# Performance work log

Hardware: AMD Instinct MI355X
Metric: run time of the kernel (lower is better)

Reference implementation:

```python
import jax, jax.numpy as jnp
import numpy as np

B, N, D, H, L, K, V = 2, 2048, 512, 8, 4, 32, 256
HD = D // H
MOD = 4294967296.0
SCALE = 1.0 / np.sqrt(HD)


def _ln(x, g, b):
    m = x.mean(-1, keepdims=True)
    v = ((x - m) ** 2).mean(-1, keepdims=True)
    return (x - m) * jax.lax.rsqrt(v + 1e-5) * g + b


def _expmap0(v, c):
    sc = jnp.sqrt(c)
    vn = jnp.maximum(jnp.linalg.norm(v, axis=-1, keepdims=True), 1e-8)
    return jnp.tanh(sc * vn) * v / (sc * vn)


def _knn_poincare(pos, c):
    xx = jnp.sum(pos ** 2, -1)                                    # [N]
    d2 = jnp.maximum(xx[:, None] + xx[None, :] - 2.0 * pos @ pos.T, 0.0)
    denom = (1.0 - c * xx)[:, None] * (1.0 - c * xx)[None, :] + 1e-8
    arg = jnp.maximum(1.0 + 2.0 * c * d2 / denom, 1.0)
    dist = jnp.arccosh(arg) / jnp.sqrt(c)                         # [N,N]
    neg_d, idx = jax.lax.top_k(-dist, K)                          # smallest-k
    return -neg_d, idx                                            # [N,K],[N,K]


def _forward(hashes, indices, emb, hash_proj, Wb, bb, log_c, pos_tangent,
             Wq, bq, Wk, bk, Wv, bv, Wo, bo, W1, b1, W2, b2,
             g1, be1, g2, be2, log_tau, Wout, bout):
    c = jnp.exp(log_c)
    char = emb[indices]                                           # [B,N,D]
    he = (hashes[..., None].astype(jnp.float32) / MOD) @ hash_proj  # [B,N,D]
    x = jnp.concatenate([char, he], -1) @ Wb + bb                 # [B,N,D]

    # kNN structure computed under no_grad in the original
    pos = _expmap0(jax.lax.stop_gradient(pos_tangent), jax.lax.stop_gradient(c))
    attn_dists, idx = _knn_poincare(pos, jax.lax.stop_gradient(c))  # shared over batch

    for i in range(L):
        xn = _ln(x, g1[i], be1[i])
        q = (xn @ Wq[i] + bq[i]).reshape(B, N, H, HD).transpose(0, 2, 1, 3)
        k = (xn @ Wk[i] + bk[i]).reshape(B, N, H, HD).transpose(0, 2, 1, 3)
        v = (xn @ Wv[i] + bv[i]).reshape(B, N, H, HD).transpose(0, 2, 1, 3)
        kg = k[:, :, idx, :]                                      # [B,H,N,K,HD]
        vg = v[:, :, idx, :]
        fs = jnp.einsum('bhnd,bhnkd->bhnk', q, kg) * SCALE
        gs = -attn_dists[None, None] / (jnp.exp(log_tau[i]) + 1e-8)
        p = jax.nn.softmax(fs + gs, axis=-1)                      # [B,H,N,K]
        ao = jnp.einsum('bhnk,bhnkd->bhnd', p, vg)
        ao = ao.transpose(0, 2, 1, 3).reshape(B, N, D)
        x = x + ao @ Wo[i] + bo[i]
        xn2 = _ln(x, g2[i], be2[i])
        x = x + jax.nn.gelu(xn2 @ W1[i] + b1[i], approximate=False) @ W2[i] + b2[i]

    return x[:, -1, :] @ Wout + bout                              # [B,V]


def setup_inputs():
    key = jax.random.key(0)
    ks = jax.random.split(key, 20)
    rn = lambda k, s, sc=0.02: jax.random.normal(k, s, jnp.float32) * sc
    z = lambda s: jnp.zeros(s, jnp.float32)
    o = lambda s: jnp.ones(s, jnp.float32)
    return {
        'hashes': jax.random.randint(ks[0], (B, N), 0, 1000000),
        'indices': jax.random.randint(ks[1], (B, N), 0, V),
        'emb': rn(ks[2], (V, D)),
        'hash_proj': rn(ks[3], (1, D)),
        'Wb': rn(ks[4], (2 * D, D)),
        'bb': z((D,)),
        'log_c': jnp.array(0.0, jnp.float32),
        'pos_tangent': rn(ks[5], (N, D)),
        'Wq': rn(ks[6], (L, D, D)), 'bq': z((L, D)),
        'Wk': rn(ks[7], (L, D, D)), 'bk': z((L, D)),
        'Wv': rn(ks[8], (L, D, D)), 'bv': z((L, D)),
        'Wo': rn(ks[9], (L, D, D)), 'bo': z((L, D)),
        'W1': rn(ks[10], (L, D, 4 * D)), 'b1': z((L, 4 * D)),
        'W2': rn(ks[11], (L, 4 * D, D)), 'b2': z((L, D)),
        'g1': o((L, D)), 'be1': z((L, D)),
        'g2': o((L, D)), 'be2': z((L, D)),
        'log_tau': z((L,)),
        'Wout': rn(ks[12], (D, V)), 'bout': z((V,)),
    }


def reference(hashes, indices, emb, hash_proj, Wb, bb, log_c, pos_tangent,
              Wq, bq, Wk, bk, Wv, bv, Wo, bo, W1, b1, W2, b2,
              g1, be1, g2, be2, log_tau, Wout, bout):
    return _forward(hashes, indices, emb, hash_proj, Wb, bb, log_c, pos_tangent,
                    Wq, bq, Wk, bk, Wv, bv, Wo, bo, W1, b1, W2, b2,
                    g1, be1, g2, be2, log_tau, Wout, bout)
```

## Files before the change

### kernel.cpp

```cpp
#include <hip/hip_runtime.h>
#include <hip/hip_bf16.h>
#include <math.h>

#define Bb 2
#define Nn 2048
#define Dd 512
#define Hh 8
#define Ll 4
#define Kk 32
#define Vv 256
#define HDh 64
#define Mrows (Bb*Nn)

static constexpr float SCALE_QK = 0.125f;
static constexpr float INV_MOD = 1.0f / 4294967296.0f;

typedef _Float16 f16;
typedef _Float16 f16x8 __attribute__((ext_vector_type(8)));
typedef _Float16 f16x4 __attribute__((ext_vector_type(4)));
typedef _Float16 f16x2 __attribute__((ext_vector_type(2)));
typedef float f32x4 __attribute__((ext_vector_type(4)));
typedef unsigned long long u64;

#define AS_GLOBAL(p) ((const __attribute__((address_space(1))) void*)(p))
#define AS_LDS(p)    ((__attribute__((address_space(3))) void*)(p))
__device__ __forceinline__ void gload16(const f16* g, f16* l) {
    __builtin_amdgcn_global_load_lds(AS_GLOBAL(g), AS_LDS(l), 16, 0, 0);
}

__global__ __launch_bounds__(256)
void prep_kernel(const float* __restrict__ log_c, const float* __restrict__ log_tau,
                 float* __restrict__ scal,
                 const float* __restrict__ bq, const float* __restrict__ bk,
                 const float* __restrict__ bv, float* __restrict__ bqkv,
                 const float* __restrict__ emb, f16* __restrict__ emb16) {
    int id = blockIdx.x * 256 + threadIdx.x;
    if (id < Vv * Dd) emb16[id] = (f16)emb[id];
    if (id < Ll * 1536) {
        int l = id / 1536, r = id % 1536;
        const float* src = (r < 512) ? bq : ((r < 1024) ? bk : bv);
        bqkv[id] = src[l * 512 + (r & 511)];
    }
    if (id == 0) {
        float c = expf(log_c[0]);
        scal[0] = c;
        scal[1] = sqrtf(c);
    }
    if (id < Ll) scal[2 + id] = 1.0f / (expf(log_tau[id]) + 1e-8f);
}

__global__ __launch_bounds__(256)
void hvec_part_kernel(const float* __restrict__ hash_proj,
                      const float* __restrict__ Wb,
                      float* __restrict__ part) {
    const int b = blockIdx.x;
    const int t = threadIdx.x;
    float a0 = 0.f, a1 = 0.f;
#pragma unroll
    for (int i = 0; i < 16; i++) {
        int kx = b * 16 + i;
        float hp = hash_proj[kx];
        const float* wr = Wb + (size_t)(Dd + kx) * Dd;
        a0 = fmaf(hp, wr[t], a0);
        a1 = fmaf(hp, wr[t + 256], a1);
    }
    part[b * Dd + t]       = a0;
    part[b * Dd + t + 256] = a1;
}
__global__ __launch_bounds__(256)
void hvec_red_kernel(const float* __restrict__ part, float* __restrict__ hvec) {
    const int n = blockIdx.x * 256 + threadIdx.x;
    float acc = 0.f;
#pragma unroll
    for (int b = 0; b < 32; b++) acc += part[b * Dd + n];
    hvec[n] = acc;
}

__global__ __launch_bounds__(256)
void trans_kernel(const float* __restrict__ src, f16* __restrict__ dst,
                  int K, int N, long sStride, long dStride) {
    __shared__ float tile[32][33];
    const float* s = src + blockIdx.z * sStride;
    f16* d = dst + blockIdx.z * dStride;
    int k0 = blockIdx.y * 32, n0 = blockIdx.x * 32;
    int tx = threadIdx.x & 31, ty = threadIdx.x >> 5;
#pragma unroll
    for (int i = 0; i < 32; i += 8)
        tile[ty + i][tx] = s[(long)(k0 + ty + i) * N + n0 + tx];
    __syncthreads();
#pragma unroll
    for (int i = 0; i < 32; i += 8)
        d[(long)(n0 + ty + i) * K + k0 + tx] = (f16)tile[tx][ty + i];
}

__global__ __launch_bounds__(256)
void trans4_kernel(const float* __restrict__ Wq, const float* __restrict__ Wk,
                   const float* __restrict__ Wv, const float* __restrict__ Wo,
                   f16* __restrict__ Wqkvt, f16* __restrict__ Wot) {
    __shared__ float tile[32][33];
    const int which = blockIdx.z >> 2, l = blockIdx.z & 3;
    const float* s;
    f16* d;
    switch (which) {
        case 0: s = Wq + (size_t)l * 262144; d = Wqkvt + (size_t)l * 786432;          break;
        case 1: s = Wk + (size_t)l * 262144; d = Wqkvt + (size_t)l * 786432 + 262144; break;
        case 2: s = Wv + (size_t)l * 262144; d = Wqkvt + (size_t)l * 786432 + 524288; break;
        default:s = Wo + (size_t)l * 262144; d = Wot   + (size_t)l * 262144;          break;
    }
    int k0 = blockIdx.y * 32, n0 = blockIdx.x * 32;
    int tx = threadIdx.x & 31, ty = threadIdx.x >> 5;
#pragma unroll
    for (int i = 0; i < 32; i += 8)
        tile[ty + i][tx] = s[(long)(k0 + ty + i) * 512 + n0 + tx];
    __syncthreads();
#pragma unroll
    for (int i = 0; i < 32; i += 8)
        d[(long)(n0 + ty + i) * 512 + k0 + tx] = (f16)tile[tx][ty + i];
}

template<int TM, int TN, bool GATHER, bool RANK1, bool GELU, bool RES, bool OUT16>
__global__ __launch_bounds__(256)
void mgemm(const f16* __restrict__ A, const f16* __restrict__ Wt,
           const float* __restrict__ bias,
           const int* __restrict__ gidx,
           const int* __restrict__ hashes, const float* __restrict__ hvec,
           const float* __restrict__ resid,
           void* __restrict__ Cout, int M, int N, int K) {
    constexpr int WRN = (TN == 64) ? 2 : 1;
    constexpr int WCN = 4 / WRN;
    constexpr int WRE = TM / WRN;
    constexpr int NIT = WRE / 16;
    constexpr int ACH = TM * 8;
    constexpr int BCH = TN * 8;
    constexpr int NCH = ACH + BCH;
    constexpr int NCHT = NCH / 256;
    constexpr int NBUF = (TN == 64) ? 3 : 2;
    static_assert(NCH % 256 == 0, "chunk count must tile the block");
    __shared__ __align__(16) f16 sm[NBUF][NCH * 8];
    const int t = threadIdx.x;
    const int lane = t & 63;
    const int w = t >> 6;
    const int wr = w / WCN, wc = w % WCN;
    const int i0 = blockIdx.y * TM, j0 = blockIdx.x * TN;

    const f16* gsrc[NCHT];
#pragma unroll
    for (int q = 0; q < NCHT; q++) {
        int c = t + q * 256;
        if (c < ACH) {
            int m = c >> 3, kb = (c & 7) ^ (m & 7);
            long row = GATHER ? (long)gidx[i0 + m] : (long)(i0 + m);
            gsrc[q] = A + row * K + kb * 8;
        } else {
            int cc = c - ACH;
            int n = cc >> 3, kb = (cc & 7) ^ (n & 7);
            gsrc[q] = Wt + (long)(j0 + n) * K + kb * 8;
        }
    }

    f32x4 acc[NIT][2];
#pragma unroll
    for (int i = 0; i < NIT; i++)
#pragma unroll
        for (int j = 0; j < 2; j++) acc[i][j] = (f32x4){0.f, 0.f, 0.f, 0.f};

    auto compute = [&](const f16* rbuf) {
#pragma unroll
        for (int kh = 0; kh < 2; kh++) {
            f16x8 af[NIT], bf[2];
#pragma unroll
            for (int i = 0; i < NIT; i++) {
                int m = wr * WRE + i * 16 + (lane & 15);
                int sl = m * 8 + ((kh * 4 + (lane >> 4)) ^ (m & 7));
                af[i] = *(const f16x8*)(rbuf + sl * 8);
            }
#pragma unroll
            for (int j = 0; j < 2; j++) {
                int n = wc * 32 + j * 16 + (lane & 15);
                int sl = ACH + n * 8 + ((kh * 4 + (lane >> 4)) ^ (n & 7));
                bf[j] = *(const f16x8*)(rbuf + sl * 8);
            }
#pragma unroll
            for (int i = 0; i < NIT; i++)
#pragma unroll
                for (int j = 0; j < 2; j++)
                    acc[i][j] = __builtin_amdgcn_mfma_f32_16x16x32_f16(af[i], bf[j], acc[i][j], 0, 0, 0);
        }
    };

    if constexpr (TN == 64) {
        static_assert(NCHT == 3 || NCHT == 4, "vmcnt immediate coverage");
        const int T = K >> 6;
#pragma unroll
        for (int q = 0; q < NCHT; q++) gload16(gsrc[q],      &sm[0][(t + q * 256) * 8]);
#pragma unroll
        for (int q = 0; q < NCHT; q++) gload16(gsrc[q] + 64, &sm[1][(t + q * 256) * 8]);
        f16 *bA = sm[0], *bB = sm[1], *bC = sm[2];
        for (int tt = 0; tt < T - 1; ++tt) {
            if constexpr (NCHT == 4) asm volatile("s_waitcnt vmcnt(4)" ::: "memory");
            else                     asm volatile("s_waitcnt vmcnt(3)" ::: "memory");
            __syncthreads();
            if (tt + 2 < T) {
                const int kt2 = (tt + 2) << 6;
#pragma unroll
                for (int q = 0; q < NCHT; q++)
                    gload16(gsrc[q] + kt2, bC + (t + q * 256) * 8);
            }
            compute(bA);
            f16* tmp = bA; bA = bB; bB = bC; bC = tmp;
        }
        asm volatile("s_waitcnt vmcnt(0)" ::: "memory");
        __syncthreads();
        compute(bA);
    } else {
#pragma unroll
        for (int q = 0; q < NCHT; q++)
            gload16(gsrc[q], &sm[0][(t + q * 256) * 8]);
        auto step = [&](int kt, const f16* rbuf, f16* wbuf) {
            asm volatile("s_waitcnt vmcnt(0)" ::: "memory");
            __syncthreads();
            if (kt + 64 < K) {
#pragma unroll
                for (int q = 0; q < NCHT; q++)
                    gload16(gsrc[q] + kt + 64, wbuf + (t + q * 256) * 8);
            }
            compute(rbuf);
        };
        for (int kt = 0; kt < K; kt += 128) {
            step(kt,      sm[0], sm[1]);
            step(kt + 64, sm[1], sm[0]);
        }
    }

    float* Cf = (float*)Cout;
    f16*   Ch = (f16*)Cout;
#pragma unroll
    for (int i = 0; i < NIT; i++) {
        int rbase = i0 + wr * WRE + i * 16 + ((lane >> 4) << 2);
#pragma unroll
        for (int v = 0; v < 4; v++) {
            int row = rbase + v;
            float hterm = RANK1 ? (float)hashes[row] * INV_MOD : 0.f;
#pragma unroll
            for (int j = 0; j < 2; j++) {
                int col = j0 + wc * 32 + j * 16 + (lane & 15);
                float val = acc[i][j][v] + bias[col];
                if (RANK1) val += hterm * hvec[col];
                if (GELU)  val = 0.5f * val * (1.f + erff(val * 0.7071067811865475f));
                if (RES)   val += resid[(long)row * N + col];
                if (OUT16) Ch[(long)row * N + col] = (f16)val;
                else       Cf[(long)row * N + col] = val;
            }
        }
    }
}

__global__ __launch_bounds__(256)
void mdist_kernel(const f16* __restrict__ poshl, const float* __restrict__ xx,
                  const float* __restrict__ scal, float* __restrict__ dist) {
    constexpr int TM = 64, TN = 64;
    constexpr int ACH = TM * 8, BCH = TN * 8, NCH = ACH + BCH;
    constexpr int NCHT = NCH / 256;
    constexpr int KK = 1024;
    __shared__ __align__(16) f16 sm[3][NCH * 8];
    const int t = threadIdx.x;
    const int lane = t & 63;
    const int w = t >> 6;
    const int wr = w >> 1, wc = w & 1;
    const int i0 = blockIdx.y * TM, j0 = blockIdx.x * TN;

    const f16* gsrc[NCHT];
#pragma unroll
    for (int q = 0; q < NCHT; q++) {
        int c = t + q * 256;
        if (c < ACH) {
            int m = c >> 3, kb = (c & 7) ^ (m & 7);
            gsrc[q] = poshl + (long)(i0 + m) * KK + kb * 8;
        } else {
            int cc = c - ACH;
            int n = cc >> 3, kb = (cc & 7) ^ (n & 7);
            gsrc[q] = poshl + (long)(j0 + n) * KK + kb * 8;
        }
    }

    f32x4 acc[2][2];
#pragma unroll
    for (int i = 0; i < 2; i++)
#pragma unroll
        for (int j = 0; j < 2; j++) acc[i][j] = (f32x4){0.f, 0.f, 0.f, 0.f};

    auto compute = [&](const f16* rbuf) {
#pragma unroll
        for (int kh = 0; kh < 2; kh++) {
            f16x8 af[2], bf[2];
#pragma unroll
            for (int i = 0; i < 2; i++) {
                int m = wr * 32 + i * 16 + (lane & 15);
                int sl = m * 8 + ((kh * 4 + (lane >> 4)) ^ (m & 7));
                af[i] = *(const f16x8*)(rbuf + sl * 8);
            }
#pragma unroll
            for (int j = 0; j < 2; j++) {
                int n = wc * 32 + j * 16 + (lane & 15);
                int sl = ACH + n * 8 + ((kh * 4 + (lane >> 4)) ^ (n & 7));
                bf[j] = *(const f16x8*)(rbuf + sl * 8);
            }
#pragma unroll
            for (int i = 0; i < 2; i++)
#pragma unroll
                for (int j = 0; j < 2; j++)
                    acc[i][j] = __builtin_amdgcn_mfma_f32_16x16x32_f16(af[i], bf[j], acc[i][j], 0, 0, 0);
        }
    };

#pragma unroll
    for (int q = 0; q < NCHT; q++) gload16(gsrc[q],      &sm[0][(t + q * 256) * 8]);
#pragma unroll
    for (int q = 0; q < NCHT; q++) gload16(gsrc[q] + 64, &sm[1][(t + q * 256) * 8]);
    f16 *bA = sm[0], *bB = sm[1], *bC = sm[2];
    constexpr int T = KK >> 6;
    for (int tt = 0; tt < T - 1; ++tt) {
        asm volatile("s_waitcnt vmcnt(4)" ::: "memory");
        __syncthreads();
        if (tt + 2 < T) {
            const int kt2 = (tt + 2) << 6;
#pragma unroll
            for (int q = 0; q < NCHT; q++)
                gload16(gsrc[q] + kt2, bC + (t + q * 256) * 8);
        }
        compute(bA);
        f16* tmp = bA; bA = bB; bB = bC; bC = tmp;
    }
    asm volatile("s_waitcnt vmcnt(0)" ::: "memory");
    __syncthreads();
    compute(bA);

    const float c = scal[0];
#pragma unroll
    for (int i = 0; i < 2; i++) {
        int rbase = i0 + wr * 32 + i * 16 + ((lane >> 4) << 2);
#pragma unroll
        for (int v = 0; v < 4; v++) {
            int row = rbase + v;
            float xi = xx[row];
#pragma unroll
            for (int j = 0; j < 2; j++) {
                int col = j0 + wc * 32 + j * 16 + (lane & 15);
                float xj = xx[col];
                float d2 = fmaxf(xi + xj - 2.f * acc[i][j][v], 0.f);
                float denom = (1.f - c * xi) * (1.f - c * xj) + 1e-8f;
                float arg = fmaxf(1.f + 2.f * c * d2 / denom, 1.f);
                dist[(long)row * Nn + col] = arg;
            }
        }
    }
}

__global__ __launch_bounds__(256)
void ln_kernel(const float* __restrict__ x, const float* __restrict__ g,
               const float* __restrict__ be, f16* __restrict__ xn) {
    const int row = blockIdx.x * 4 + (threadIdx.x >> 6);
    const int t = threadIdx.x & 63;
    const float4* xr = (const float4*)(x + (size_t)row * Dd);
    float4 v0 = xr[t], v1 = xr[t + 64];
    float s = v0.x + v0.y + v0.z + v0.w + v1.x + v1.y + v1.z + v1.w;
#pragma unroll
    for (int off = 32; off; off >>= 1) s += __shfl_xor(s, off, 64);
    float mean = s * (1.f / Dd);
    float d0x = v0.x - mean, d0y = v0.y - mean, d0z = v0.z - mean, d0w = v0.w - mean;
    float d1x = v1.x - mean, d1y = v1.y - mean, d1z = v1.z - mean, d1w = v1.w - mean;
    float q = d0x*d0x + d0y*d0y + d0z*d0z + d0w*d0w
            + d1x*d1x + d1y*d1y + d1z*d1z + d1w*d1w;
#pragma unroll
    for (int off = 32; off; off >>= 1) q += __shfl_xor(q, off, 64);
    float rstd = rsqrtf(q * (1.f / Dd) + 1e-5f);
    float4 g0 = ((const float4*)g)[t], g1v = ((const float4*)g)[t + 64];
    float4 b0 = ((const float4*)be)[t], b1v = ((const float4*)be)[t + 64];
    f16* xo = xn + (size_t)row * Dd;
    f16x4 o0, o1;
    o0[0] = (f16)(d0x * rstd * g0.x + b0.x);
    o0[1] = (f16)(d0y * rstd * g0.y + b0.y);
    o0[2] = (f16)(d0z * rstd * g0.z + b0.z);
    o0[3] = (f16)(d0w * rstd * g0.w + b0.w);
    o1[0] = (f16)(d1x * rstd * g1v.x + b1v.x);
    o1[1] = (f16)(d1y * rstd * g1v.y + b1v.y);
    o1[2] = (f16)(d1z * rstd * g1v.z + b1v.z);
    o1[3] = (f16)(d1w * rstd * g1v.w + b1v.w);
    *(f16x4*)(xo + t * 4)         = o0;
    *(f16x4*)(xo + (t + 64) * 4)  = o1;
}

__global__ __launch_bounds__(256)
void expmap_kernel(const float* __restrict__ vt, const float* __restrict__ scal,
                   f16* __restrict__ poshl, float* __restrict__ xx) {
    __shared__ float red[256];
    const int row = blockIdx.x, t = threadIdx.x;
    const float* vr = vt + (size_t)row * Dd;
    float v0 = vr[t], v1 = vr[t + 256];
    red[t] = v0 * v0 + v1 * v1;
    __syncthreads();
    for (int off = 128; off; off >>= 1) {
        if (t < off) red[t] += red[t + off];
        __syncthreads();
    }
    float total = red[0];
    float vn = fmaxf(sqrtf(total), 1e-8f);
    float sc = scal[1];
    float factor = tanhf(sc * vn) / (sc * vn);
    float p0 = factor * v0, p1 = factor * v1;
    f16 h0 = (f16)p0, h1 = (f16)p1;
    f16* pr = poshl + (size_t)row * 1024;
    pr[t]             = h0;
    pr[t + 256]       = h1;
    pr[512 + t]       = (f16)(p0 - (float)h0);
    pr[512 + t + 256] = (f16)(p1 - (float)h1);
    if (t == 0) xx[row] = factor * factor * total;
}

__global__ __launch_bounds__(256)
void topk_kernel(const float* __restrict__ dist, const float* __restrict__ scal,
                 float* __restrict__ outd, int* __restrict__ outi) {
    __shared__ unsigned wred[4];
    __shared__ unsigned bc;
    __shared__ __align__(8) u64 buf[128];
    const int t = threadIdx.x;
    const int w = t >> 6;
    const int n = blockIdx.x;
    const float sqc = scal[1];
    const uint4* dr = (const uint4*)(dist + (size_t)n * Nn);

    uint4 va = dr[t * 2];
    uint4 vb = dr[t * 2 + 1];
    unsigned k[8] = {va.x, va.y, va.z, va.w, vb.x, vb.y, vb.z, vb.w};
    const int g0 = t * 8;

    unsigned lo = 0x3F800000u;
    unsigned hi = 0x7F800001u;
    unsigned chi = 2048u;
    while (chi > 96u && (hi - lo) > 1u) {
        unsigned mid = lo + ((hi - lo) >> 1);
        int c = 0;
#pragma unroll
        for (int j = 0; j < 8; j++) c += (k[j] < mid) ? 1 : 0;
#pragma unroll
        for (int off = 32; off; off >>= 1) c += __shfl_xor(c, off, 64);
        __syncthreads();
        if ((t & 63) == 0) wred[w] = (unsigned)c;
        __syncthreads();
        unsigned ct = wred[0] + wred[1] + wred[2] + wred[3];
        if (ct >= 32u) { hi = mid; chi = ct; } else { lo = mid; }
    }

    if (chi <= 96u) {
        if (t == 0) bc = 0u;
        __syncthreads();
#pragma unroll
        for (int j = 0; j < 8; j++) {
            if (k[j] < hi) {
                unsigned s = atomicAdd(&bc, 1u);
                buf[s] = ((u64)k[j] << 11) | (u64)(unsigned)(g0 + j);
            }
        }
        __syncthreads();
        const int m = (int)chi;
        if (t < m) {
            u64 my = buf[t];
            int r = 0;
            for (int j = 0; j < m; j++) r += (buf[j] < my) ? 1 : 0;
            if (r < Kk) {
                float v = __uint_as_float((unsigned)(my >> 11));
                outd[n * Kk + r] = acoshf(v) / sqc;
                outi[n * Kk + r] = (int)(my & 2047u);
            }
        }
    } else {
        int c = 0;
#pragma unroll
        for (int j = 0; j < 8; j++) c += (k[j] < lo) ? 1 : 0;
#pragma unroll
        for (int off = 32; off; off >>= 1) c += __shfl_xor(c, off, 64);
        __syncthreads();
        if ((t & 63) == 0) wred[w] = (unsigned)c;
        if (t == 0) bc = 0u;
        __syncthreads();
        const int cless = (int)(wred[0] + wred[1] + wred[2] + wred[3]);
#pragma unroll
        for (int j = 0; j < 8; j++) {
            if (k[j] < lo) {
                unsigned s = atomicAdd(&bc, 1u);
                buf[s] = ((u64)k[j] << 11) | (u64)(unsigned)(g0 + j);
            }
        }
        __syncthreads();
        if (t < cless) {
            u64 my = buf[t];
            int r = 0;
            for (int j = 0; j < cless; j++) r += (buf[j] < my) ? 1 : 0;
            float v = __uint_as_float((unsigned)(my >> 11));
            outd[n * Kk + r] = acoshf(v) / sqc;
            outi[n * Kk + r] = (int)(my & 2047u);
        }
        const int need = Kk - cless;
        unsigned eqm = 0u;
#pragma unroll
        for (int j = 0; j < 8; j++) if (k[j] == lo) eqm |= (1u << j);
        const float dv = acoshf(__uint_as_float(lo)) / sqc;
        for (int s = 0; s < need; s++) {
            int mi = 0x7FFFFFFF;
#pragma unroll
            for (int j = 0; j < 8; j++)
                if (eqm & (1u << j)) mi = min(mi, g0 + j);
#pragma unroll
            for (int off = 32; off; off >>= 1) mi = min(mi, __shfl_xor(mi, off, 64));
            __syncthreads();
            if ((t & 63) == 0) wred[w] = (unsigned)mi;
            __syncthreads();
            int m4 = (int)min(min(wred[0], wred[1]), min(wred[2], wred[3]));
            int j = m4 - g0;
            if (j >= 0 && j < 8 && (eqm & (1u << j))) {
                eqm &= ~(1u << j);
                outd[n * Kk + cless + s] = dv;
                outi[n * Kk + cless + s] = m4;
            }
        }
    }
}

#define KSTR 520
__global__ __launch_bounds__(256)
void attn_kernel(const f16* __restrict__ qkv, const float* __restrict__ adist,
                 const int* __restrict__ aidx, const float* __restrict__ scal,
                 int layer, f16* __restrict__ ao) {
    __shared__ __align__(16) f16 ks[Kk * KSTR];
    __shared__ float ps[Hh][Kk];
    __shared__ int   sidx[Kk];
    const int t = threadIdx.x;
    const int b = blockIdx.x >> 11, n = blockIdx.x & (Nn - 1);
    const float inv_tau = scal[2 + layer];
    const int h = t >> 5, j = t & 31;

    if (t < Kk) sidx[t] = aidx[n * Kk + t];
#pragma unroll
    for (int q = 0; q < 8; q++) {
        int c = q * 256 + t;
        int jr = c >> 6, ci = c & 63;
        int row = aidx[n * Kk + jr];
        *(f16x8*)(ks + jr * KSTR + ci * 8) =
            *(const f16x8*)(qkv + (size_t)(b * Nn + row) * 1536 + 512 + ci * 8);
    }
    __syncthreads();

    const f16* qrow = qkv + (size_t)(b * Nn + n) * 1536 + h * HDh;
    float dot = 0.f;
#pragma unroll
    for (int i = 0; i < 8; i++) {
        f16x8 qa = *(const f16x8*)(qrow + i * 8);
        f16x8 ka = *(const f16x8*)(ks + j * KSTR + h * HDh + i * 8);
#pragma unroll
        for (int m = 0; m < 4; m++) {
            f16x2 qp = {qa[2 * m], qa[2 * m + 1]};
            f16x2 kp = {ka[2 * m], ka[2 * m + 1]};
            dot = __builtin_amdgcn_fdot2(qp, kp, dot, false);
        }
    }
    float s = dot * SCALE_QK - adist[n * Kk + j] * inv_tau;
    float mx = s;
#pragma unroll
    for (int off = 16; off; off >>= 1) mx = fmaxf(mx, __shfl_xor(mx, off, 64));
    float e = expf(s - mx);
    float sum = e;
#pragma unroll
    for (int off = 16; off; off >>= 1) sum += __shfl_xor(sum, off, 64);
    ps[h][j] = e / sum;
    __syncthreads();

    const int d2 = t & 31;
    const size_t voff = 1024 + (size_t)h * HDh + d2 * 2;
    float a0 = 0.f, a1 = 0.f;
#pragma unroll
    for (int jj = 0; jj < Kk; jj++) {
        float p = ps[h][jj];
        f16x2 vv = *(const f16x2*)(qkv + (size_t)(b * Nn + sidx[jj]) * 1536 + voff);
        a0 = fmaf(p, (float)vv[0], a0);
        a1 = fmaf(p, (float)vv[1], a1);
    }
    f16x2 outv; outv[0] = (f16)a0; outv[1] = (f16)a1;
    *(f16x2*)(ao + (size_t)(b * Nn + n) * Dd + h * HDh + d2 * 2) = outv;
}

__global__ __launch_bounds__(1024)
void out_kernel(const float* __restrict__ x, const float* __restrict__ Wout,
                const float* __restrict__ bout, float* __restrict__ out) {
    __shared__ float red[3][256];
    const int b = blockIdx.x;
    const int g = threadIdx.x >> 8, vc = threadIdx.x & 255;
    const float* xr = x + ((size_t)(b * Nn + (Nn - 1))) * Dd;
    float acc = 0.f;
    for (int d = g * 128; d < (g + 1) * 128; d++)
        acc = fmaf(xr[d], Wout[(size_t)d * Vv + vc], acc);
    if (g) red[g - 1][vc] = acc;
    __syncthreads();
    if (g == 0)
        out[b * Vv + vc] = acc + red[0][vc] + red[1][vc] + red[2][vc] + bout[vc];
}

static constexpr size_t X_OFF     = 0;
static constexpr size_t XN16_OFF  = 8388608;
static constexpr size_t QKV16_OFF = 12582912;
static constexpr size_t AO16_OFF  = 25165824;
static constexpr size_t H1_OFF    = 29360128;
static constexpr size_t AD_OFF    = 46137344;
static constexpr size_t AI_OFF    = 46399488;
static constexpr size_t SC_OFF    = 46661632;
static constexpr size_t HV_OFF    = 46661888;
static constexpr size_t XX_OFF    = 46663936;
static constexpr size_t BQKV_OFF  = 46672128;
static constexpr size_t EMB16_OFF = 46704896;
static constexpr size_t WBT_OFF   = 46967040;
static constexpr size_t WQKVT_OFF = 47491328;
static constexpr size_t WOT_OFF   = 53782784;
static constexpr size_t W1T_OFF   = 55879936;
static constexpr size_t W2T_OFF   = 64268544;
static constexpr size_t HP_OFF    = 72657152;

extern "C" void kernel_launch(void* const* d_in, const int* in_sizes, int n_in,
                              void* d_out, int out_size, void* d_ws, size_t ws_size,
                              hipStream_t stream) {
    (void)in_sizes; (void)n_in; (void)out_size; (void)ws_size;
    const int*   hashes    = (const int*)  d_in[0];
    const int*   indices   = (const int*)  d_in[1];
    const float* emb       = (const float*)d_in[2];
    const float* hash_proj = (const float*)d_in[3];
    const float* Wb        = (const float*)d_in[4];
    const float* bb        = (const float*)d_in[5];
    const float* log_c     = (const float*)d_in[6];
    const float* pos_t     = (const float*)d_in[7];
    const float* Wq        = (const float*)d_in[8];
    const float* bq        = (const float*)d_in[9];
    const float* Wk        = (const float*)d_in[10];
    const float* bk        = (const float*)d_in[11];
    const float* Wv        = (const float*)d_in[12];
    const float* bv        = (const float*)d_in[13];
    const float* Wo        = (const float*)d_in[14];
    const float* bo        = (const float*)d_in[15];
    const float* W1        = (const float*)d_in[16];
    const float* b1        = (const float*)d_in[17];
    const float* W2        = (const float*)d_in[18];
    const float* b2        = (const float*)d_in[19];
    const float* g1        = (const float*)d_in[20];
    const float* be1       = (const float*)d_in[21];
    const float* g2        = (const float*)d_in[22];
    const float* be2       = (const float*)d_in[23];
    const float* log_tau   = (const float*)d_in[24];
    const float* Wout      = (const float*)d_in[25];
    const float* bout      = (const float*)d_in[26];

    char* ws = (char*)d_ws;
    float* x      = (float*)(ws + X_OFF);
    f16*   xn16   = (f16*)  (ws + XN16_OFF);
    f16*   qkv16  = (f16*)  (ws + QKV16_OFF);
    f16*   ao16   = (f16*)  (ws + AO16_OFF);
    f16*   h1     = (f16*)  (ws + H1_OFF);
    float* adist  = (float*)(ws + AD_OFF);
    int*   aidx   = (int*)  (ws + AI_OFF);
    float* scal   = (float*)(ws + SC_OFF);
    float* hvec   = (float*)(ws + HV_OFF);
    float* xxb    = (float*)(ws + XX_OFF);
    float* bqkv   = (float*)(ws + BQKV_OFF);
    f16*   emb16  = (f16*)  (ws + EMB16_OFF);
    f16*   Wbt    = (f16*)  (ws + WBT_OFF);
    f16*   Wqkvt  = (f16*)  (ws + WQKVT_OFF);
    f16*   Wot    = (f16*)  (ws + WOT_OFF);
    f16*   W1t    = (f16*)  (ws + W1T_OFF);
    f16*   W2t    = (f16*)  (ws + W2T_OFF);
    float* hpart  = (float*)(ws + HP_OFF);
    f16*   poshl  = (f16*)  (ws + AO16_OFF);
    float* distb  = (float*)(ws + H1_OFF);

    prep_kernel<<<512, 256, 0, stream>>>(log_c, log_tau, scal, bq, bk, bv, bqkv, emb, emb16);
    hvec_part_kernel<<<32, 256, 0, stream>>>(hash_proj, Wb, hpart);
    hvec_red_kernel<<<2, 256, 0, stream>>>(hpart, hvec);
    trans_kernel<<<dim3(16, 16, 1), 256, 0, stream>>>(Wb, Wbt, 512, 512, 0, 0);
    trans4_kernel<<<dim3(16, 16, 16), 256, 0, stream>>>(Wq, Wk, Wv, Wo, Wqkvt, Wot);
    trans_kernel<<<dim3(64, 16, Ll), 256, 0, stream>>>(W1, W1t, 512, 2048, 1048576, 1048576);
    trans_kernel<<<dim3(16, 64, Ll), 256, 0, stream>>>(W2, W2t, 2048, 512, 1048576, 1048576);

    mgemm<32, 64, true, true, false, false, false><<<dim3(8, 128), 256, 0, stream>>>(
        emb16, Wbt, bb, indices, hashes, hvec, nullptr, x, Mrows, Dd, Dd);

    expmap_kernel<<<Nn, 256, 0, stream>>>(pos_t, scal, poshl, xxb);
    mdist_kernel<<<dim3(32, 32), 256, 0, stream>>>(poshl, xxb, scal, distb);
    topk_kernel<<<Nn, 256, 0, stream>>>(distb, scal, adist, aidx);

    for (int l = 0; l < Ll; l++) {
        ln_kernel<<<Mrows / 4, 256, 0, stream>>>(x, g1 + l * Dd, be1 + l * Dd, xn16);
        mgemm<64, 128, false, false, false, false, true><<<dim3(12, 64), 256, 0, stream>>>(
            xn16, Wqkvt + (size_t)l * 786432, bqkv + l * 1536,
            nullptr, nullptr, nullptr, nullptr, qkv16, Mrows, 1536, Dd);
        attn_kernel<<<Bb * Nn, 256, 0, stream>>>(qkv16, adist, aidx, scal, l, ao16);
        mgemm<32, 64, false, false, false, true, false><<<dim3(8, 128), 256, 0, stream>>>(
            ao16, Wot + (size_t)l * 262144, bo + l * Dd,
            nullptr, nullptr, nullptr, x, x, Mrows, Dd, Dd);
        ln_kernel<<<Mrows / 4, 256, 0, stream>>>(x, g2 + l * Dd, be2 + l * Dd, xn16);
        mgemm<64, 128, false, false, true, false, true><<<dim3(16, 64), 256, 0, stream>>>(
            xn16, W1t + (size_t)l * 1048576, b1 + l * 4 * Dd,
            nullptr, nullptr, nullptr, nullptr, h1, Mrows, 4 * Dd, Dd);
        mgemm<32, 64, false, false, false, true, false><<<dim3(8, 128), 256, 0, stream>>>(
            h1, W2t + (size_t)l * 1048576, b2 + l * Dd,
            nullptr, nullptr, nullptr, x, x, Mrows, Dd, 4 * Dd);
    }

    out_kernel<<<Bb, 1024, 0, stream>>>(x, Wout, bout, (float*)d_out);
}
```

Before: 572.2 us.

## Exploit distance symmetry, enlarge FFN GEMM tiles, hoist query loads in attention

The Poincare distance kernel now launches only upper-triangular 64x64 tiles (528 blocks) and writes each off-diagonal tile twice, once directly and once transposed through shared memory. This roughly halves the matmul work for the symmetric distance matrix. The FFN GEMMs switch to 128-row tiles with a generalized warp layout and per-warp column count, so each staged tile is reused more but there are fewer blocks. The W2 GEMM now uses 6 loads per thread and a matching vmcnt wait, and attention loads q and the distance value before the barrier.

```diff
diff --git a/kernel.cpp b/kernel.cpp
--- a/kernel.cpp
+++ b/kernel.cpp
@@ -126,10 +126,12 @@
            const int* __restrict__ hashes, const float* __restrict__ hvec,
            const float* __restrict__ resid,
            void* __restrict__ Cout, int M, int N, int K) {
-    constexpr int WRN = (TN == 64) ? 2 : 1;
+    constexpr int WRN = (TN == 64) ? 2 : ((TM == 128) ? 2 : 1);
     constexpr int WCN = 4 / WRN;
     constexpr int WRE = TM / WRN;
     constexpr int NIT = WRE / 16;
+    constexpr int COLE = TN / WCN;
+    constexpr int NJT = COLE / 16;
     constexpr int ACH = TM * 8;
     constexpr int BCH = TN * 8;
     constexpr int NCH = ACH + BCH;
@@ -158,16 +160,16 @@
         }
     }
 
-    f32x4 acc[NIT][2];
+    f32x4 acc[NIT][NJT];
 #pragma unroll
     for (int i = 0; i < NIT; i++)
 #pragma unroll
-        for (int j = 0; j < 2; j++) acc[i][j] = (f32x4){0.f, 0.f, 0.f, 0.f};
+        for (int j = 0; j < NJT; j++) acc[i][j] = (f32x4){0.f, 0.f, 0.f, 0.f};
 
     auto compute = [&](const f16* rbuf) {
 #pragma unroll
         for (int kh = 0; kh < 2; kh++) {
-            f16x8 af[NIT], bf[2];
+            f16x8 af[NIT], bf[NJT];
 #pragma unroll
             for (int i = 0; i < NIT; i++) {
                 int m = wr * WRE + i * 16 + (lane & 15);
@@ -175,21 +177,21 @@
                 af[i] = *(const f16x8*)(rbuf + sl * 8);
             }
 #pragma unroll
-            for (int j = 0; j < 2; j++) {
-                int n = wc * 32 + j * 16 + (lane & 15);
+            for (int j = 0; j < NJT; j++) {
+                int n = wc * COLE + j * 16 + (lane & 15);
                 int sl = ACH + n * 8 + ((kh * 4 + (lane >> 4)) ^ (n & 7));
                 bf[j] = *(const f16x8*)(rbuf + sl * 8);
             }
 #pragma unroll
             for (int i = 0; i < NIT; i++)
 #pragma unroll
-                for (int j = 0; j < 2; j++)
+                for (int j = 0; j < NJT; j++)
                     acc[i][j] = __builtin_amdgcn_mfma_f32_16x16x32_f16(af[i], bf[j], acc[i][j], 0, 0, 0);
         }
     };
 
     if constexpr (TN == 64) {
-        static_assert(NCHT == 3 || NCHT == 4, "vmcnt immediate coverage");
+        static_assert(NCHT == 3 || NCHT == 4 || NCHT == 6, "vmcnt immediate coverage");
         const int T = K >> 6;
 #pragma unroll
         for (int q = 0; q < NCHT; q++) gload16(gsrc[q],      &sm[0][(t + q * 256) * 8]);
@@ -197,8 +199,9 @@
         for (int q = 0; q < NCHT; q++) gload16(gsrc[q] + 64, &sm[1][(t + q * 256) * 8]);
         f16 *bA = sm[0], *bB = sm[1], *bC = sm[2];
         for (int tt = 0; tt < T - 1; ++tt) {
-            if constexpr (NCHT == 4) asm volatile("s_waitcnt vmcnt(4)" ::: "memory");
-            else                     asm volatile("s_waitcnt vmcnt(3)" ::: "memory");
+            if constexpr (NCHT == 3)      asm volatile("s_waitcnt vmcnt(3)" ::: "memory");
+            else if constexpr (NCHT == 4) asm volatile("s_waitcnt vmcnt(4)" ::: "memory");
+            else                          asm volatile("s_waitcnt vmcnt(6)" ::: "memory");
             __syncthreads();
             if (tt + 2 < T) {
                 const int kt2 = (tt + 2) << 6;
@@ -242,8 +245,8 @@
             int row = rbase + v;
             float hterm = RANK1 ? (float)hashes[row] * INV_MOD : 0.f;
 #pragma unroll
-            for (int j = 0; j < 2; j++) {
-                int col = j0 + wc * 32 + j * 16 + (lane & 15);
+            for (int j = 0; j < NJT; j++) {
+                int col = j0 + wc * COLE + j * 16 + (lane & 15);
                 float val = acc[i][j][v] + bias[col];
                 if (RANK1) val += hterm * hvec[col];
                 if (GELU)  val = 0.5f * val * (1.f + erff(val * 0.7071067811865475f));
@@ -267,7 +270,13 @@
     const int lane = t & 63;
     const int w = t >> 6;
     const int wr = w >> 1, wc = w & 1;
-    const int i0 = blockIdx.y * TM, j0 = blockIdx.x * TN;
+
+    const int bi = blockIdx.x;
+    int r = (int)((65.0f - sqrtf(4225.0f - 8.0f * (float)bi)) * 0.5f);
+    while (32 * (r + 1) - ((r + 1) * r) / 2 <= bi) r++;
+    while (32 * r - (r * (r - 1)) / 2 > bi) r--;
+    const int by = r, bx = r + (bi - (32 * r - (r * (r - 1)) / 2));
+    const int i0 = by * TM, j0 = bx * TN;
 
     const f16* gsrc[NCHT];
 #pragma unroll
@@ -336,6 +345,7 @@
     compute(bA);
 
     const float c = scal[0];
+    float vals[2][4][2];
 #pragma unroll
     for (int i = 0; i < 2; i++) {
         int rbase = i0 + wr * 32 + i * 16 + ((lane >> 4) << 2);
@@ -350,8 +360,37 @@
                 float d2 = fmaxf(xi + xj - 2.f * acc[i][j][v], 0.f);
                 float denom = (1.f - c * xi) * (1.f - c * xj) + 1e-8f;
                 float arg = fmaxf(1.f + 2.f * c * d2 / denom, 1.f);
+                vals[i][v][j] = arg;
                 dist[(long)row * Nn + col] = arg;
             }
+        }
+    }
+    if (bx != by) {
+        __syncthreads();
+        float* trf = (float*)sm;
+#pragma unroll
+        for (int i = 0; i < 2; i++) {
+#pragma unroll
+            for (int v = 0; v < 4; v++) {
+                int rw = wr * 32 + i * 16 + ((lane >> 4) << 2) + v;
+#pragma unroll
+                for (int j = 0; j < 2; j++) {
+                    int cl = wc * 32 + j * 16 + (lane & 15);
+                    trf[cl * 65 + rw] = vals[i][v][j];
+                }
+            }
+        }
+        __syncthreads();
+        const int cl = t >> 2, q4 = t & 3;
+#pragma unroll
+        for (int s = 0; s < 4; s++) {
+            int rw = q4 * 16 + s * 4;
+            float4 wv;
+            wv.x = trf[cl * 65 + rw];
+            wv.y = trf[cl * 65 + rw + 1];
+            wv.z = trf[cl * 65 + rw + 2];
+            wv.w = trf[cl * 65 + rw + 3];
+            *(float4*)(dist + (long)(j0 + cl) * Nn + i0 + rw) = wv;
         }
     }
 }
@@ -539,6 +578,12 @@
     const float inv_tau = scal[2 + layer];
     const int h = t >> 5, j = t & 31;
 
+    const f16* qrow = qkv + (size_t)(b * Nn + n) * 1536 + h * HDh;
+    f16x8 qa[8];
+#pragma unroll
+    for (int i = 0; i < 8; i++) qa[i] = *(const f16x8*)(qrow + i * 8);
+    const float sd = adist[n * Kk + j];
+
     if (t < Kk) sidx[t] = aidx[n * Kk + t];
 #pragma unroll
     for (int q = 0; q < 8; q++) {
@@ -550,20 +595,18 @@
     }
     __syncthreads();
 
-    const f16* qrow = qkv + (size_t)(b * Nn + n) * 1536 + h * HDh;
     float dot = 0.f;
 #pragma unroll
     for (int i = 0; i < 8; i++) {
-        f16x8 qa = *(const f16x8*)(qrow + i * 8);
         f16x8 ka = *(const f16x8*)(ks + j * KSTR + h * HDh + i * 8);
 #pragma unroll
         for (int m = 0; m < 4; m++) {
-            f16x2 qp = {qa[2 * m], qa[2 * m + 1]};
+            f16x2 qp = {qa[i][2 * m], qa[i][2 * m + 1]};
             f16x2 kp = {ka[2 * m], ka[2 * m + 1]};
             dot = __builtin_amdgcn_fdot2(qp, kp, dot, false);
         }
     }
-    float s = dot * SCALE_QK - adist[n * Kk + j] * inv_tau;
+    float s = dot * SCALE_QK - sd * inv_tau;
     float mx = s;
 #pragma unroll
     for (int off = 16; off; off >>= 1) mx = fmaxf(mx, __shfl_xor(mx, off, 64));
@@ -689,7 +732,7 @@
         emb16, Wbt, bb, indices, hashes, hvec, nullptr, x, Mrows, Dd, Dd);
 
     expmap_kernel<<<Nn, 256, 0, stream>>>(pos_t, scal, poshl, xxb);
-    mdist_kernel<<<dim3(32, 32), 256, 0, stream>>>(poshl, xxb, scal, distb);
+    mdist_kernel<<<528, 256, 0, stream>>>(poshl, xxb, scal, distb);
     topk_kernel<<<Nn, 256, 0, stream>>>(distb, scal, adist, aidx);
 
     for (int l = 0; l < Ll; l++) {
@@ -702,10 +745,10 @@
             ao16, Wot + (size_t)l * 262144, bo + l * Dd,
             nullptr, nullptr, nullptr, x, x, Mrows, Dd, Dd);
         ln_kernel<<<Mrows / 4, 256, 0, stream>>>(x, g2 + l * Dd, be2 + l * Dd, xn16);
-        mgemm<64, 128, false, false, true, false, true><<<dim3(16, 64), 256, 0, stream>>>(
+        mgemm<128, 128, false, false, true, false, true><<<dim3(16, 32), 256, 0, stream>>>(
             xn16, W1t + (size_t)l * 1048576, b1 + l * 4 * Dd,
             nullptr, nullptr, nullptr, nullptr, h1, Mrows, 4 * Dd, Dd);
-        mgemm<32, 64, false, false, false, true, false><<<dim3(8, 128), 256, 0, stream>>>(
+        mgemm<128, 64, false, false, false, true, false><<<dim3(8, 32), 256, 0, stream>>>(
             h1, W2t + (size_t)l * 1048576, b2 + l * Dd,
             nullptr, nullptr, nullptr, x, x, Mrows, Dd, 4 * Dd);
     }
```

Result: slower. 591.1 us (+3.3%).
